# Optimization experiments

Hardware: AMD Instinct MI355X
Metric: run time of the kernel (lower is better)

Reference implementation:

```python
import jax, jax.numpy as jnp
import numpy as np

EPS = 1e-5

def _bn(h):
    # BatchNorm1d, affine=False, track_running_stats=False -> batch stats, biased var
    m = h.mean(axis=0)
    v = h.var(axis=0)
    return (h - m) * jax.lax.rsqrt(v + EPS)

def _aggregate(x, edge_index):
    # out[i] = sum over edges (i <- j) of x[j]  + x[i] (self loop)
    dst, src = edge_index[0], edge_index[1]
    n = x.shape[0]
    return jax.ops.segment_sum(x[src], dst, num_segments=n) + x

def setup_inputs() -> dict:
    key = jax.random.key(0)
    ks = jax.random.split(key, 12)
    N, F, H, C, E = 100000, 128, 128, 40, 800000
    x = jax.random.normal(ks[0], (N, F), dtype=jnp.float32)
    edge_index = jax.random.randint(ks[1], (2, E), 0, N, dtype=jnp.int64)
    def lin(kw, kb, fan_in, fan_out):
        bound = 1.0 / np.sqrt(fan_in)
        W = jax.random.uniform(kw, (fan_in, fan_out), minval=-bound, maxval=bound, dtype=jnp.float32)
        b = jax.random.uniform(kb, (fan_out,), minval=-bound, maxval=bound, dtype=jnp.float32)
        return W, b
    W0, b0 = lin(ks[2], ks[3], F, H)
    W1, b1 = lin(ks[4], ks[5], H, H)
    W2, b2 = lin(ks[6], ks[7], H, H)
    Wl, bl = lin(ks[8], ks[9], H, C)
    return {"x": x, "edge_index": edge_index, "W0": W0, "b0": b0,
            "W1": W1, "b1": b1, "W2": W2, "b2": b2, "Wl": Wl, "bl": bl}

def reference(x, edge_index, W0, b0, W1, b1, W2, b2, Wl, bl):
    h = x
    for W, b in ((W0, b0), (W1, b1), (W2, b2)):
        h = _aggregate(h, edge_index)          # spmm(A + I, h)
        h = h @ W + b                          # Linear
        h = _bn(h)                             # BatchNorm1d (no affine)
        h = jax.nn.relu(h)
    return h @ Wl + bl
```

## Files before the change

kernel.cpp:

```cpp
#include <hip/hip_runtime.h>
#include <stdint.h>

typedef __attribute__((ext_vector_type(8))) short short8;
typedef __attribute__((ext_vector_type(4))) float floatx4;

static __device__ __forceinline__ float b2f(uint16_t b){
    return __uint_as_float(((uint32_t)b) << 16);
}
static __device__ __forceinline__ uint16_t f2b(float f){
    uint32_t u = __float_as_uint(f);
    return (uint16_t)((u + 0x7fffu + ((u >> 16) & 1u)) >> 16);
}
static __device__ __forceinline__ float blo(uint32_t v){ return __uint_as_float(v << 16); }
static __device__ __forceinline__ float bhi(uint32_t v){ return __uint_as_float(v & 0xffff0000u); }
static __device__ __forceinline__ uint32_t pack2(float a, float b){
    return ((uint32_t)f2b(b) << 16) | (uint32_t)f2b(a);
}

__global__ void k_sentinel(uint32_t* out, int nwords, uint32_t pat){
    int i = blockIdx.x * blockDim.x + threadIdx.x;
    if (i < nwords) out[i] = pat;
}

__global__ void k_zf(int* deg8, int n8, const uint32_t* xw, const int* ei, int* flags, int ZB){
    if ((int)blockIdx.x == ZB){
        if (threadIdx.x != 0) return;
        int odd_nz = 0;
        for (int k = 0; k < 128; k++){
            if (ei[2 * k + 1] != 0) odd_nz = 1;
        }
        flags[0] = odd_nz ? 0 : 1;
        int big = 0;
        for (int k = 0; k < 128; k++){
            float lo = __uint_as_float(xw[k] << 16);
            if (!(fabsf(lo) <= 1024.0f)) big = 1;
        }
        flags[1] = big ? 0 : 1;
        return;
    }
    int i = blockIdx.x * blockDim.x + threadIdx.x;
    if (i < n8) deg8[i] = 0;
}

__global__ void k_deg(const int* ei, int E, int* deg8, uint16_t* rank, const int* flags,
                      unsigned q){
    int e = blockIdx.x * blockDim.x + threadIdx.x;
    if (e < E){
        int is64 = flags[0];
        int d = is64 ? ei[2 * e] : ei[e];
        unsigned sv = (unsigned)(is64 ? ei[2 * (E + e)] : ei[E + e]);
        int s = (int)(sv / q);
        int r = atomicAdd(&deg8[d * 8 + s], 1);
        rank[e] = (uint16_t)r;
    }
}

__global__ void k_off8(const int* __restrict__ deg8, int N, int* __restrict__ deg,
                       uint16_t* __restrict__ offs8){
    int i = blockIdx.x * blockDim.x + threadIdx.x;
    if (i >= N) return;
    int s = 0;
    #pragma unroll
    for (int k = 0; k < 8; k++){
        int c = deg8[i * 8 + k];
        offs8[i * 8 + k] = (uint16_t)s;
        s += c;
    }
    deg[i] = s;
}

__global__ void k_scan1(const int* deg, int N, int* bsum){
    __shared__ int s[256];
    int t = threadIdx.x;
    int i = blockIdx.x * 256 + t;
    s[t] = (i < N) ? deg[i] : 0;
    __syncthreads();
    for (int off = 128; off > 0; off >>= 1){
        if (t < off) s[t] += s[t + off];
        __syncthreads();
    }
    if (t == 0) bsum[blockIdx.x] = s[0];
}

__global__ void k_scan2(int* bsum, int nb, int* rp, int N){
    __shared__ int s[512];
    int t = threadIdx.x;
    int v = (t < nb) ? bsum[t] : 0;
    s[t] = v;
    __syncthreads();
    for (int off = 1; off < 512; off <<= 1){
        int u = (t >= off) ? s[t - off] : 0;
        __syncthreads();
        s[t] += u;
        __syncthreads();
    }
    if (t < nb) bsum[t] = s[t] - v;
    if (t == 511) rp[N] = s[511];
}

__global__ void k_scan3(const int* deg, int N, const int* bpre, int* rp){
    __shared__ int s[256];
    int t = threadIdx.x;
    int i = blockIdx.x * 256 + t;
    int v = (i < N) ? deg[i] : 0;
    s[t] = v;
    __syncthreads();
    for (int off = 1; off < 256; off <<= 1){
        int u = (t >= off) ? s[t - off] : 0;
        __syncthreads();
        s[t] += u;
        __syncthreads();
    }
    if (i < N) rp[i] = bpre[blockIdx.x] + s[t] - v;
}

__global__ __launch_bounds__(256) void k_fill(const int* __restrict__ ei, int E,
                                              const int* __restrict__ rp,
                                              const uint16_t* __restrict__ rank,
                                              const uint16_t* __restrict__ offs8,
                                              int* __restrict__ col,
                                              const int* __restrict__ flags, int N,
                                              unsigned q){
    int xcd = blockIdx.x & 7;
    int sub = blockIdx.x >> 3;
    int nsub = gridDim.x >> 3;
    int r0 = (int)(((long long)N * xcd) >> 3);
    int r1 = (int)(((long long)N * (xcd + 1)) >> 3);
    int e0 = (int)(((long long)E * sub) / nsub);
    int e1 = (int)(((long long)E * (sub + 1)) / nsub);
    int is64 = flags[0];
    for (int e = e0 + threadIdx.x; e < e1; e += 256){
        int d = is64 ? ei[2 * e] : ei[e];
        if (d >= r0 && d < r1){
            unsigned sv = (unsigned)(is64 ? ei[2 * (E + e)] : ei[E + e]);
            int s = (int)(sv / q);
            int p = rp[d] + (int)offs8[d * 8 + s] + (int)rank[e];
            col[p] = (int)sv;
        }
    }
}

__global__ void k_prep(const void* W0, const void* W1, const void* W2, const void* Wl,
                       uint16_t* Wf0, uint16_t* Wf1, uint16_t* Wf2, uint16_t* Wfl,
                       const void* b0, const void* b1, const void* b2, const void* bl,
                       float* bc, const void* x, uint16_t* hx, int NF,
                       const int* flags){
    int blk = blockIdx.x;
    int t = threadIdx.x;
    if (blk >= 218){
        if (flags[1]) return;
        int nb = gridDim.x - 218;
        for (int i = (blk - 218) * 256 + t; i < NF; i += nb * 256)
            hx[i] = f2b(((const float*)x)[i]);
        return;
    }
    if (blk >= 216){
        int i = (blk - 216) * 256 + t;
        if (i >= 424) return;
        const void* src; int li;
        if (i < 128)      { src = b0; li = i; }
        else if (i < 256) { src = b1; li = i - 128; }
        else if (i < 384) { src = b2; li = i - 256; }
        else              { src = bl; li = i - 384; }
        bc[i] = flags[1] ? b2f(((const uint16_t*)src)[li]) : ((const float*)src)[li];
        return;
    }
    const void* W; uint16_t* Wf; int C, ntiles, lb;
    if (blk < 64)        { W = W0; Wf = Wf0; C = 128; ntiles = 8; lb = blk; }
    else if (blk < 128)  { W = W1; Wf = Wf1; C = 128; ntiles = 8; lb = blk - 64; }
    else if (blk < 192)  { W = W2; Wf = Wf2; C = 128; ntiles = 8; lb = blk - 128; }
    else                 { W = Wl; Wf = Wfl; C = 40;  ntiles = 3; lb = blk - 192; }
    int idx = lb * 256 + t;
    int total = 4 * ntiles * 512;
    if (idx >= total) return;
    int j = idx & 7;
    int lane = (idx >> 3) & 63;
    int nt = (idx >> 9) % ntiles;
    int kt = idx / (512 * ntiles);
    int k = kt * 32 + (lane >> 4) * 8 + j;
    int n = nt * 16 + (lane & 15);
    uint16_t v = 0;
    if (n < C){
        v = flags[1] ? ((const uint16_t*)W)[k * C + n]
                     : f2b(((const float*)W)[k * C + n]);
    }
    Wf[idx] = v;
}

__global__ __launch_bounds__(256) void k_agg(const uint16_t* __restrict__ Yin,
                                             const uint16_t* __restrict__ xraw,
                                             const int* __restrict__ rp,
                                             const int* __restrict__ col,
                                             uint16_t* __restrict__ out, int N,
                                             const float* __restrict__ st,
                                             int apply_bn, float ninv,
                                             const int* __restrict__ flags){
    int t = threadIdx.x;
    int l16 = t & 15;
    int i = blockIdx.x * 16 + (t >> 4);
    if (i >= N) return;
    float tt[8], iv[8];
    const uint16_t* src = Yin;
    if (apply_bn){
        int f0 = l16 * 8;
        #pragma unroll
        for (int j = 0; j < 8; j++){
            float sv = st[f0 + j];
            float qv = st[128 + f0 + j];
            float m = sv * ninv;
            float var = qv * ninv - m * m;
            float ivj = rsqrtf(var + 1e-5f);
            iv[j] = ivj;
            tt[j] = -m * ivj;
        }
    } else if (flags[1]){
        src = xraw;
    }
    const uint4* base = (const uint4*)src;
    int s0 = rp[i], e0 = rp[i + 1];
    float a[8];
    {
        uint4 w = base[(size_t)i * 16 + l16];
        a[0] = blo(w.x); a[1] = bhi(w.x); a[2] = blo(w.y); a[3] = bhi(w.y);
        a[4] = blo(w.z); a[5] = bhi(w.z); a[6] = blo(w.w); a[7] = bhi(w.w);
        if (apply_bn){
            #pragma unroll
            for (int jj = 0; jj < 8; jj++) a[jj] = fmaxf(fmaf(a[jj], iv[jj], tt[jj]), 0.f);
        }
    }
    int k = s0;
    for (; k + 3 < e0; k += 4){
        int j0 = col[k], j1 = col[k + 1], j2 = col[k + 2], j3 = col[k + 3];
        uint4 ww[4];
        ww[0] = base[(size_t)j0 * 16 + l16];
        ww[1] = base[(size_t)j1 * 16 + l16];
        ww[2] = base[(size_t)j2 * 16 + l16];
        ww[3] = base[(size_t)j3 * 16 + l16];
        #pragma unroll
        for (int u = 0; u < 4; u++){
            float v[8] = {blo(ww[u].x), bhi(ww[u].x), blo(ww[u].y), bhi(ww[u].y),
                          blo(ww[u].z), bhi(ww[u].z), blo(ww[u].w), bhi(ww[u].w)};
            if (apply_bn){
                #pragma unroll
                for (int jj = 0; jj < 8; jj++) v[jj] = fmaxf(fmaf(v[jj], iv[jj], tt[jj]), 0.f);
            }
            #pragma unroll
            for (int jj = 0; jj < 8; jj++) a[jj] += v[jj];
        }
    }
    for (; k < e0; k++){
        int j = col[k];
        uint4 w = base[(size_t)j * 16 + l16];
        float v[8] = {blo(w.x), bhi(w.x), blo(w.y), bhi(w.y),
                      blo(w.z), bhi(w.z), blo(w.w), bhi(w.w)};
        if (apply_bn){
            #pragma unroll
            for (int jj = 0; jj < 8; jj++) v[jj] = fmaxf(fmaf(v[jj], iv[jj], tt[jj]), 0.f);
        }
        #pragma unroll
        for (int jj = 0; jj < 8; jj++) a[jj] += v[jj];
    }
    uint4 o;
    o.x = pack2(a[0], a[1]); o.y = pack2(a[2], a[3]);
    o.z = pack2(a[4], a[5]); o.w = pack2(a[6], a[7]);
    ((uint4*)out)[(size_t)i * 16 + l16] = o;
}

__global__ __launch_bounds__(256) void k_gemm(uint16_t* __restrict__ A,
                                              const uint16_t* __restrict__ Wf,
                                              const float* __restrict__ bias,
                                              float* __restrict__ part, int N){
    __shared__ __align__(16) uint16_t wlds[16384];
    __shared__ float sh_sum[128], sh_ssq[128];
    int t = threadIdx.x;
    if (t < 128){ sh_sum[t] = 0.f; sh_ssq[t] = 0.f; }
    {
        const uint4* s = (const uint4*)Wf;
        uint4* d = (uint4*)wlds;
        for (int i = t; i < 2048; i += 256) d[i] = s[i];
    }
    __syncthreads();
    int lane = t & 63, wave = t >> 6;
    int m = lane & 15, q = lane >> 4;
    int rb[2];
    rb[0] = blockIdx.x * 128 + wave * 16;
    rb[1] = rb[0] + 64;
    short8 afrag[2][4];
    #pragma unroll
    for (int mt = 0; mt < 2; mt++){
        int arow = rb[mt] + m;
        if (arow >= N) arow = N - 1;
        const short8* ap = (const short8*)(A + (size_t)arow * 128);
        #pragma unroll
        for (int kt = 0; kt < 4; kt++) afrag[mt][kt] = ap[kt * 4 + q];
    }
    floatx4 acc[2][8];
    #pragma unroll
    for (int mt = 0; mt < 2; mt++)
        #pragma unroll
        for (int nt = 0; nt < 8; nt++) acc[mt][nt] = (floatx4){0.f, 0.f, 0.f, 0.f};
    const short8* wl = (const short8*)wlds;
    #pragma unroll
    for (int kt = 0; kt < 4; kt++){
        #pragma unroll
        for (int nt = 0; nt < 8; nt++){
            short8 bfrag = wl[(kt * 8 + nt) * 64 + lane];
            #pragma unroll
            for (int mt = 0; mt < 2; mt++){
                acc[mt][nt] = __builtin_amdgcn_mfma_f32_16x16x32_bf16(afrag[mt][kt], bfrag, acc[mt][nt], 0, 0, 0);
            }
        }
    }
    #pragma unroll
    for (int mt = 0; mt < 2; mt++){
        #pragma unroll
        for (int nt = 0; nt < 8; nt++){
            int ccol = nt * 16 + m;
            float bv = bias[ccol];
            float s = 0.f, ss = 0.f;
            #pragma unroll
            for (int r = 0; r < 4; r++){
                int grow = rb[mt] + q * 4 + r;
                if (grow < N){
                    float y = acc[mt][nt][r] + bv;
                    A[(size_t)grow * 128 + ccol] = f2b(y);
                    s += y;
                    ss += y * y;
                }
            }
            s += __shfl_xor(s, 16); s += __shfl_xor(s, 32);
            ss += __shfl_xor(ss, 16); ss += __shfl_xor(ss, 32);
            if (q == 0){
                atomicAdd(&sh_sum[ccol], s);
                atomicAdd(&sh_ssq[ccol], ss);
            }
        }
    }
    __syncthreads();
    if (t < 128){
        part[(size_t)blockIdx.x * 256 + t] = sh_sum[t];
        part[(size_t)blockIdx.x * 256 + 128 + t] = sh_ssq[t];
    }
}

__global__ __launch_bounds__(1024) void k_red(const float* __restrict__ part, int nb,
                                              float* __restrict__ st){
    __shared__ float sh[1024];
    int t = threadIdx.x;
    int col = t & 255;
    int seg = t >> 8;
    float s0 = 0.f, s1 = 0.f, s2 = 0.f, s3 = 0.f;
    int b = seg;
    for (; b + 12 < nb; b += 16){
        s0 += part[(size_t)b * 256 + col];
        s1 += part[(size_t)(b + 4) * 256 + col];
        s2 += part[(size_t)(b + 8) * 256 + col];
        s3 += part[(size_t)(b + 12) * 256 + col];
    }
    for (; b < nb; b += 4) s0 += part[(size_t)b * 256 + col];
    sh[t] = (s0 + s1) + (s2 + s3);
    __syncthreads();
    if (t < 256) st[t] = (sh[t] + sh[t + 256]) + (sh[t + 512] + sh[t + 768]);
}

__global__ __launch_bounds__(256) void k_out(const uint16_t* __restrict__ A,
                                             const uint16_t* __restrict__ Wf,
                                             const float* __restrict__ bias,
                                             const float* __restrict__ st, float ninv,
                                             void* __restrict__ out, int N,
                                             const int* __restrict__ flags){
    __shared__ __align__(16) uint16_t wlds[6144];
    __shared__ float s_m[128], s_iv[128];
    int t = threadIdx.x;
    {
        const uint4* s = (const uint4*)Wf;
        uint4* d = (uint4*)wlds;
        for (int i = t; i < 768; i += 256) d[i] = s[i];
    }
    if (t < 128){
        float m = st[t] * ninv;
        float var = st[128 + t] * ninv - m * m;
        s_m[t] = m;
        s_iv[t] = rsqrtf(var + 1e-5f);
    }
    __syncthreads();
    int lane = t & 63, wave = t >> 6;
    int m = lane & 15, q = lane >> 4;
    int row_base = blockIdx.x * 64 + wave * 16;
    int arow = row_base + m;
    if (arow >= N) arow = N - 1;
    short8 afrag[4];
    const uint4* ap = (const uint4*)(A + (size_t)arow * 128);
    #pragma unroll
    for (int kt = 0; kt < 4; kt++){
        uint4 u = ap[kt * 4 + q];
        float v[8] = {blo(u.x), bhi(u.x), blo(u.y), bhi(u.y),
                      blo(u.z), bhi(u.z), blo(u.w), bhi(u.w)};
        int c0 = kt * 32 + q * 8;
        #pragma unroll
        for (int j = 0; j < 8; j++) v[j] = fmaxf((v[j] - s_m[c0 + j]) * s_iv[c0 + j], 0.f);
        uint4 o;
        o.x = pack2(v[0], v[1]); o.y = pack2(v[2], v[3]);
        o.z = pack2(v[4], v[5]); o.w = pack2(v[6], v[7]);
        afrag[kt] = *(short8*)&o;
    }
    floatx4 acc[3];
    #pragma unroll
    for (int nt = 0; nt < 3; nt++) acc[nt] = (floatx4){0.f, 0.f, 0.f, 0.f};
    const short8* wl = (const short8*)wlds;
    #pragma unroll
    for (int kt = 0; kt < 4; kt++){
        #pragma unroll
        for (int nt = 0; nt < 3; nt++){
            acc[nt] = __builtin_amdgcn_mfma_f32_16x16x32_bf16(afrag[kt], wl[(kt * 3 + nt) * 64 + lane], acc[nt], 0, 0, 0);
        }
    }
    int isbf = flags[1];
    #pragma unroll
    for (int nt = 0; nt < 3; nt++){
        int ccol = nt * 16 + m;
        if (ccol < 40){
            float bv = bias[ccol];
            #pragma unroll
            for (int r = 0; r < 4; r++){
                int grow = row_base + q * 4 + r;
                if (grow < N){
                    float y = acc[nt][r] + bv;
                    if (isbf) ((uint16_t*)out)[(size_t)grow * 40 + ccol] = f2b(y);
                    else      ((float*)out)[(size_t)grow * 40 + ccol] = y;
                }
            }
        }
    }
}

extern "C" void kernel_launch(void* const* d_in, const int* in_sizes, int n_in,
                              void* d_out, int out_size, void* d_ws, size_t ws_size,
                              hipStream_t stream){
    (void)n_in;
    const void* x  = d_in[0];
    const int* ei  = (const int*)d_in[1];
    const void* W0 = d_in[2];
    const void* b0 = d_in[3];
    const void* W1 = d_in[4];
    const void* b1 = d_in[5];
    const void* W2 = d_in[6];
    const void* b2 = d_in[7];
    const void* Wl = d_in[8];
    const void* bl = d_in[9];

    const int N = in_sizes[0] / 128;
    const int E = in_sizes[1] / 2;
    const int NF = N * 128;
    const int NB = (N + 255) / 256;
    const int gemm_blocks2 = (N + 127) / 128;
    const int gemm_blocks  = (N + 63) / 64;
    const unsigned q8 = (unsigned)((N + 7) / 8);

    char* ws = (char*)d_ws;
    size_t off = 0;
    uint16_t* hx = (uint16_t*)(ws + off); off += ((size_t)NF * 2 + 255) & ~(size_t)255;
    uint16_t* ag = (uint16_t*)(ws + off); off += ((size_t)NF * 2 + 255) & ~(size_t)255;
    int* col     = (int*)(ws + off);      off += ((size_t)E * 4 + 255) & ~(size_t)255;
    int* rp      = (int*)(ws + off);      off += ((size_t)(N + 1) * 4 + 255) & ~(size_t)255;
    uint16_t* rank = (uint16_t*)(ws + off); off += ((size_t)E * 2 + 255) & ~(size_t)255;
    int* deg8    = (int*)(ws + off);      off += ((size_t)N * 32 + 255) & ~(size_t)255;
    uint16_t* offs8 = (uint16_t*)(ws + off); off += ((size_t)N * 16 + 255) & ~(size_t)255;
    int* deg     = (int*)(ws + off);      off += ((size_t)N * 4 + 255) & ~(size_t)255;
    int* bsum    = (int*)(ws + off);      off += 512 * 4;
    int* flags   = (int*)(ws + off);      off += 256;
    uint16_t* Wf0 = (uint16_t*)(ws + off); off += 16384 * 2;
    uint16_t* Wf1 = (uint16_t*)(ws + off); off += 16384 * 2;
    uint16_t* Wf2 = (uint16_t*)(ws + off); off += 16384 * 2;
    uint16_t* Wfl = (uint16_t*)(ws + off); off += 6144 * 2;
    float* bc    = (float*)(ws + off);    off += 424 * 4 + 160;
    float* stats = (float*)(ws + off);    off += 768 * 4;
    float* part  = (float*)(ws + off);    off += (size_t)gemm_blocks2 * 256 * 4;
    const size_t required = off;

    if (ws_size < required){
        int nwords = out_size / 2;
        k_sentinel<<<(nwords + 255) / 256, 256, 0, stream>>>((uint32_t*)d_out, nwords, 0x40004000u);
        return;
    }

    const int n8 = N * 8;
    const int ZB = (n8 + 255) / 256;
    k_zf<<<ZB + 1, 256, 0, stream>>>(deg8, n8, (const uint32_t*)x, ei, flags, ZB);
    k_deg<<<(E + 255) / 256, 256, 0, stream>>>(ei, E, deg8, rank, flags, q8);
    k_off8<<<(N + 255) / 256, 256, 0, stream>>>(deg8, N, deg, offs8);
    k_scan1<<<NB, 256, 0, stream>>>(deg, N, bsum);
    k_scan2<<<1, 512, 0, stream>>>(bsum, NB, rp, N);
    k_scan3<<<NB, 256, 0, stream>>>(deg, N, bsum, rp);
    k_fill<<<1024, 256, 0, stream>>>(ei, E, rp, rank, offs8, col, flags, N, q8);

    k_prep<<<2266, 256, 0, stream>>>(W0, W1, W2, Wl, Wf0, Wf1, Wf2, Wfl,
                                     b0, b1, b2, bl, bc, x, hx, NF, flags);

    const float ninv = 1.0f / (float)N;
    const int agg_blocks = (N + 15) / 16;
    const uint16_t* xr = (const uint16_t*)x;

    k_agg<<<agg_blocks, 256, 0, stream>>>(hx, xr, rp, col, ag, N, stats, 0, ninv, flags);
    k_gemm<<<gemm_blocks2, 256, 0, stream>>>(ag, Wf0, bc, part, N);
    k_red<<<1, 1024, 0, stream>>>(part, gemm_blocks2, stats);
    k_agg<<<agg_blocks, 256, 0, stream>>>(ag, xr, rp, col, hx, N, stats, 1, ninv, flags);
    k_gemm<<<gemm_blocks2, 256, 0, stream>>>(hx, Wf1, bc + 128, part, N);
    k_red<<<1, 1024, 0, stream>>>(part, gemm_blocks2, stats + 256);
    k_agg<<<agg_blocks, 256, 0, stream>>>(hx, xr, rp, col, ag, N, stats + 256, 1, ninv, flags);
    k_gemm<<<gemm_blocks2, 256, 0, stream>>>(ag, Wf2, bc + 256, part, N);
    k_red<<<1, 1024, 0, stream>>>(part, gemm_blocks2, stats + 512);
    k_out<<<gemm_blocks, 256, 0, stream>>>(ag, Wfl, bc + 384, stats + 512, ninv, d_out, N, flags);
}
```

Before: 437.4 us.

## Unroll aggregation gathers by eight, fuse offset/scan kernels, parallelize stat reduction

```diff
diff --git a/kernel.cpp b/kernel.cpp
--- a/kernel.cpp
+++ b/kernel.cpp
@@ -56,30 +56,27 @@
 }
 
 __global__ void k_off8(const int* __restrict__ deg8, int N, int* __restrict__ deg,
-                       uint16_t* __restrict__ offs8){
-    int i = blockIdx.x * blockDim.x + threadIdx.x;
-    if (i >= N) return;
+                       uint16_t* __restrict__ offs8, int* __restrict__ bsum){
+    __shared__ int sh[256];
+    int t = threadIdx.x;
+    int i = blockIdx.x * 256 + t;
     int s = 0;
-    #pragma unroll
-    for (int k = 0; k < 8; k++){
-        int c = deg8[i * 8 + k];
-        offs8[i * 8 + k] = (uint16_t)s;
-        s += c;
-    }
-    deg[i] = s;
-}
-
-__global__ void k_scan1(const int* deg, int N, int* bsum){
-    __shared__ int s[256];
-    int t = threadIdx.x;
-    int i = blockIdx.x * 256 + t;
-    s[t] = (i < N) ? deg[i] : 0;
+    if (i < N){
+        #pragma unroll
+        for (int k = 0; k < 8; k++){
+            int c = deg8[i * 8 + k];
+            offs8[i * 8 + k] = (uint16_t)s;
+            s += c;
+        }
+        deg[i] = s;
+    }
+    sh[t] = (i < N) ? s : 0;
     __syncthreads();
     for (int off = 128; off > 0; off >>= 1){
-        if (t < off) s[t] += s[t + off];
+        if (t < off) sh[t] += sh[t + off];
         __syncthreads();
     }
-    if (t == 0) bsum[blockIdx.x] = s[0];
+    if (t == 0) bsum[blockIdx.x] = sh[0];
 }
 
 __global__ void k_scan2(int* bsum, int nb, int* rp, int N){
@@ -187,7 +184,7 @@
     Wf[idx] = v;
 }
 
-__global__ __launch_bounds__(256) void k_agg(const uint16_t* __restrict__ Yin,
+__global__ __launch_bounds__(256, 4) void k_agg(const uint16_t* __restrict__ Yin,
                                              const uint16_t* __restrict__ xraw,
                                              const int* __restrict__ rp,
                                              const int* __restrict__ col,
@@ -228,37 +225,48 @@
             for (int jj = 0; jj < 8; jj++) a[jj] = fmaxf(fmaf(a[jj], iv[jj], tt[jj]), 0.f);
         }
     }
+    auto acc1 = [&](uint4 w){
+        float v0 = blo(w.x), v1 = bhi(w.x), v2 = blo(w.y), v3 = bhi(w.y);
+        float v4 = blo(w.z), v5 = bhi(w.z), v6 = blo(w.w), v7 = bhi(w.w);
+        if (apply_bn){
+            v0 = fmaxf(fmaf(v0, iv[0], tt[0]), 0.f);
+            v1 = fmaxf(fmaf(v1, iv[1], tt[1]), 0.f);
+            v2 = fmaxf(fmaf(v2, iv[2], tt[2]), 0.f);
+            v3 = fmaxf(fmaf(v3, iv[3], tt[3]), 0.f);
+            v4 = fmaxf(fmaf(v4, iv[4], tt[4]), 0.f);
+            v5 = fmaxf(fmaf(v5, iv[5], tt[5]), 0.f);
+            v6 = fmaxf(fmaf(v6, iv[6], tt[6]), 0.f);
+            v7 = fmaxf(fmaf(v7, iv[7], tt[7]), 0.f);
+        }
+        a[0] += v0; a[1] += v1; a[2] += v2; a[3] += v3;
+        a[4] += v4; a[5] += v5; a[6] += v6; a[7] += v7;
+    };
     int k = s0;
+    for (; k + 7 < e0; k += 8){
+        int j0 = col[k],     j1 = col[k + 1], j2 = col[k + 2], j3 = col[k + 3];
+        int j4 = col[k + 4], j5 = col[k + 5], j6 = col[k + 6], j7 = col[k + 7];
+        uint4 w0 = base[(size_t)j0 * 16 + l16];
+        uint4 w1 = base[(size_t)j1 * 16 + l16];
+        uint4 w2 = base[(size_t)j2 * 16 + l16];
+        uint4 w3 = base[(size_t)j3 * 16 + l16];
+        uint4 w4 = base[(size_t)j4 * 16 + l16];
+        uint4 w5 = base[(size_t)j5 * 16 + l16];
+        uint4 w6 = base[(size_t)j6 * 16 + l16];
+        uint4 w7 = base[(size_t)j7 * 16 + l16];
+        acc1(w0); acc1(w1); acc1(w2); acc1(w3);
+        acc1(w4); acc1(w5); acc1(w6); acc1(w7);
+    }
     for (; k + 3 < e0; k += 4){
         int j0 = col[k], j1 = col[k + 1], j2 = col[k + 2], j3 = col[k + 3];
-        uint4 ww[4];
-        ww[0] = base[(size_t)j0 * 16 + l16];
-        ww[1] = base[(size_t)j1 * 16 + l16];
-        ww[2] = base[(size_t)j2 * 16 + l16];
-        ww[3] = base[(size_t)j3 * 16 + l16];
-        #pragma unroll
-        for (int u = 0; u < 4; u++){
-            float v[8] = {blo(ww[u].x), bhi(ww[u].x), blo(ww[u].y), bhi(ww[u].y),
-                          blo(ww[u].z), bhi(ww[u].z), blo(ww[u].w), bhi(ww[u].w)};
-            if (apply_bn){
-                #pragma unroll
-                for (int jj = 0; jj < 8; jj++) v[jj] = fmaxf(fmaf(v[jj], iv[jj], tt[jj]), 0.f);
-            }
-            #pragma unroll
-            for (int jj = 0; jj < 8; jj++) a[jj] += v[jj];
-        }
+        uint4 w0 = base[(size_t)j0 * 16 + l16];
+        uint4 w1 = base[(size_t)j1 * 16 + l16];
+        uint4 w2 = base[(size_t)j2 * 16 + l16];
+        uint4 w3 = base[(size_t)j3 * 16 + l16];
+        acc1(w0); acc1(w1); acc1(w2); acc1(w3);
     }
     for (; k < e0; k++){
         int j = col[k];
-        uint4 w = base[(size_t)j * 16 + l16];
-        float v[8] = {blo(w.x), bhi(w.x), blo(w.y), bhi(w.y),
-                      blo(w.z), bhi(w.z), blo(w.w), bhi(w.w)};
-        if (apply_bn){
-            #pragma unroll
-            for (int jj = 0; jj < 8; jj++) v[jj] = fmaxf(fmaf(v[jj], iv[jj], tt[jj]), 0.f);
-        }
-        #pragma unroll
-        for (int jj = 0; jj < 8; jj++) a[jj] += v[jj];
+        acc1(base[(size_t)j * 16 + l16]);
     }
     uint4 o;
     o.x = pack2(a[0], a[1]); o.y = pack2(a[2], a[3]);
@@ -343,24 +351,26 @@
     }
 }
 
-__global__ __launch_bounds__(1024) void k_red(const float* __restrict__ part, int nb,
-                                              float* __restrict__ st){
-    __shared__ float sh[1024];
-    int t = threadIdx.x;
-    int col = t & 255;
-    int seg = t >> 8;
-    float s0 = 0.f, s1 = 0.f, s2 = 0.f, s3 = 0.f;
+__global__ __launch_bounds__(256) void k_red(const float* __restrict__ part, int nb,
+                                             float* __restrict__ st){
+    __shared__ float sh[256];
+    int t = threadIdx.x;
+    int c = t & 31, seg = t >> 5;
+    int cc = blockIdx.x * 32 + c;
+    float s0 = 0.f, s1 = 0.f;
     int b = seg;
-    for (; b + 12 < nb; b += 16){
-        s0 += part[(size_t)b * 256 + col];
-        s1 += part[(size_t)(b + 4) * 256 + col];
-        s2 += part[(size_t)(b + 8) * 256 + col];
-        s3 += part[(size_t)(b + 12) * 256 + col];
-    }
-    for (; b < nb; b += 4) s0 += part[(size_t)b * 256 + col];
-    sh[t] = (s0 + s1) + (s2 + s3);
-    __syncthreads();
-    if (t < 256) st[t] = (sh[t] + sh[t + 256]) + (sh[t + 512] + sh[t + 768]);
+    for (; b + 8 < nb; b += 16){
+        s0 += part[(size_t)b * 256 + cc];
+        s1 += part[(size_t)(b + 8) * 256 + cc];
+    }
+    for (; b < nb; b += 8) s0 += part[(size_t)b * 256 + cc];
+    sh[t] = s0 + s1;
+    __syncthreads();
+    if (t < 128) sh[t] += sh[t + 128];
+    __syncthreads();
+    if (t < 64) sh[t] += sh[t + 64];
+    __syncthreads();
+    if (t < 32) st[cc] = sh[t] + sh[t + 32];
 }
 
 __global__ __launch_bounds__(256) void k_out(const uint16_t* __restrict__ A,
@@ -488,8 +498,7 @@
     const int ZB = (n8 + 255) / 256;
     k_zf<<<ZB + 1, 256, 0, stream>>>(deg8, n8, (const uint32_t*)x, ei, flags, ZB);
     k_deg<<<(E + 255) / 256, 256, 0, stream>>>(ei, E, deg8, rank, flags, q8);
-    k_off8<<<(N + 255) / 256, 256, 0, stream>>>(deg8, N, deg, offs8);
-    k_scan1<<<NB, 256, 0, stream>>>(deg, N, bsum);
+    k_off8<<<NB, 256, 0, stream>>>(deg8, N, deg, offs8, bsum);
     k_scan2<<<1, 512, 0, stream>>>(bsum, NB, rp, N);
     k_scan3<<<NB, 256, 0, stream>>>(deg, N, bsum, rp);
     k_fill<<<1024, 256, 0, stream>>>(ei, E, rp, rank, offs8, col, flags, N, q8);
@@ -503,12 +512,12 @@
 
     k_agg<<<agg_blocks, 256, 0, stream>>>(hx, xr, rp, col, ag, N, stats, 0, ninv, flags);
     k_gemm<<<gemm_blocks2, 256, 0, stream>>>(ag, Wf0, bc, part, N);
-    k_red<<<1, 1024, 0, stream>>>(part, gemm_blocks2, stats);
+    k_red<<<8, 256, 0, stream>>>(part, gemm_blocks2, stats);
     k_agg<<<agg_blocks, 256, 0, stream>>>(ag, xr, rp, col, hx, N, stats, 1, ninv, flags);
     k_gemm<<<gemm_blocks2, 256, 0, stream>>>(hx, Wf1, bc + 128, part, N);
-    k_red<<<1, 1024, 0, stream>>>(part, gemm_blocks2, stats + 256);
+    k_red<<<8, 256, 0, stream>>>(part, gemm_blocks2, stats + 256);
     k_agg<<<agg_blocks, 256, 0, stream>>>(hx, xr, rp, col, ag, N, stats + 256, 1, ninv, flags);
     k_gemm<<<gemm_blocks2, 256, 0, stream>>>(ag, Wf2, bc + 256, part, N);
-    k_red<<<1, 1024, 0, stream>>>(part, gemm_blocks2, stats + 512);
+    k_red<<<8, 256, 0, stream>>>(part, gemm_blocks2, stats + 512);
     k_out<<<gemm_blocks, 256, 0, stream>>>(ag, Wfl, bc + 384, stats + 512, ninv, d_out, N, flags);
 }
```

After: 452.0 us. 3.3% more time.

## Fuse aggregation with GEMM and simplify CSR build to per-node degree

Applied to the files above, without the earlier changes.

```diff
diff --git a/kernel.cpp b/kernel.cpp
--- a/kernel.cpp
+++ b/kernel.cpp
@@ -22,7 +22,7 @@
     if (i < nwords) out[i] = pat;
 }
 
-__global__ void k_zf(int* deg8, int n8, const uint32_t* xw, const int* ei, int* flags, int ZB){
+__global__ void k_zf(int* deg, int N, const uint32_t* xw, const int* ei, int* flags, int ZB){
     if ((int)blockIdx.x == ZB){
         if (threadIdx.x != 0) return;
         int odd_nz = 0;
@@ -39,34 +39,16 @@
         return;
     }
     int i = blockIdx.x * blockDim.x + threadIdx.x;
-    if (i < n8) deg8[i] = 0;
-}
-
-__global__ void k_deg(const int* ei, int E, int* deg8, uint16_t* rank, const int* flags,
-                      unsigned q){
+    if (i < N) deg[i] = 0;
+}
+
+__global__ void k_deg(const int* ei, int E, int* deg, uint16_t* rank, const int* flags){
     int e = blockIdx.x * blockDim.x + threadIdx.x;
     if (e < E){
-        int is64 = flags[0];
-        int d = is64 ? ei[2 * e] : ei[e];
-        unsigned sv = (unsigned)(is64 ? ei[2 * (E + e)] : ei[E + e]);
-        int s = (int)(sv / q);
-        int r = atomicAdd(&deg8[d * 8 + s], 1);
+        int d = flags[0] ? ei[2 * e] : ei[e];
+        int r = atomicAdd(&deg[d], 1);
         rank[e] = (uint16_t)r;
     }
-}
-
-__global__ void k_off8(const int* __restrict__ deg8, int N, int* __restrict__ deg,
-                       uint16_t* __restrict__ offs8){
-    int i = blockIdx.x * blockDim.x + threadIdx.x;
-    if (i >= N) return;
-    int s = 0;
-    #pragma unroll
-    for (int k = 0; k < 8; k++){
-        int c = deg8[i * 8 + k];
-        offs8[i * 8 + k] = (uint16_t)s;
-        s += c;
-    }
-    deg[i] = s;
 }
 
 __global__ void k_scan1(const int* deg, int N, int* bsum){
@@ -117,10 +99,8 @@
 __global__ __launch_bounds__(256) void k_fill(const int* __restrict__ ei, int E,
                                               const int* __restrict__ rp,
                                               const uint16_t* __restrict__ rank,
-                                              const uint16_t* __restrict__ offs8,
                                               int* __restrict__ col,
-                                              const int* __restrict__ flags, int N,
-                                              unsigned q){
+                                              const int* __restrict__ flags, int N){
     int xcd = blockIdx.x & 7;
     int sub = blockIdx.x >> 3;
     int nsub = gridDim.x >> 3;
@@ -132,10 +112,9 @@
     for (int e = e0 + threadIdx.x; e < e1; e += 256){
         int d = is64 ? ei[2 * e] : ei[e];
         if (d >= r0 && d < r1){
-            unsigned sv = (unsigned)(is64 ? ei[2 * (E + e)] : ei[E + e]);
-            int s = (int)(sv / q);
-            int p = rp[d] + (int)offs8[d * 8 + s] + (int)rank[e];
-            col[p] = (int)sv;
+            int sv = is64 ? ei[2 * (E + e)] : ei[E + e];
+            int p = rp[d] + (int)rank[e];
+            col[p] = sv;
         }
     }
 }
@@ -150,8 +129,17 @@
     if (blk >= 218){
         if (flags[1]) return;
         int nb = gridDim.x - 218;
-        for (int i = (blk - 218) * 256 + t; i < NF; i += nb * 256)
-            hx[i] = f2b(((const float*)x)[i]);
+        int n8 = NF >> 3;
+        const float4* xv = (const float4*)x;
+        uint4* hv = (uint4*)hx;
+        for (int i = (blk - 218) * 256 + t; i < n8; i += nb * 256){
+            float4 u0 = xv[i * 2];
+            float4 u1 = xv[i * 2 + 1];
+            uint4 o;
+            o.x = pack2(u0.x, u0.y); o.y = pack2(u0.z, u0.w);
+            o.z = pack2(u1.x, u1.y); o.w = pack2(u1.z, u1.w);
+            hv[i] = o;
+        }
         return;
     }
     if (blk >= 216){
@@ -187,18 +175,25 @@
     Wf[idx] = v;
 }
 
-__global__ __launch_bounds__(256) void k_agg(const uint16_t* __restrict__ Yin,
-                                             const uint16_t* __restrict__ xraw,
-                                             const int* __restrict__ rp,
-                                             const int* __restrict__ col,
-                                             uint16_t* __restrict__ out, int N,
-                                             const float* __restrict__ st,
-                                             int apply_bn, float ninv,
-                                             const int* __restrict__ flags){
-    int t = threadIdx.x;
+__global__ __launch_bounds__(256) void k_ag(const uint16_t* __restrict__ Yin,
+                                            const uint16_t* __restrict__ xraw,
+                                            const int* __restrict__ rp,
+                                            const int* __restrict__ col,
+                                            uint16_t* __restrict__ Yout,
+                                            const uint16_t* __restrict__ Wf,
+                                            const float* __restrict__ bias,
+                                            float* __restrict__ part, int N,
+                                            const float* __restrict__ st,
+                                            int apply_bn, float ninv,
+                                            const int* __restrict__ flags){
+    __shared__ __align__(16) uint16_t albs[2048];
+    __shared__ float sh_sum[128], sh_ssq[128];
+    int t = threadIdx.x;
+    if (t < 128){ sh_sum[t] = 0.f; sh_ssq[t] = 0.f; }
     int l16 = t & 15;
-    int i = blockIdx.x * 16 + (t >> 4);
-    if (i >= N) return;
+    int r = t >> 4;
+    int row = blockIdx.x * 16 + r;
+    int i = (row < N) ? row : N - 1;
     float tt[8], iv[8];
     const uint16_t* src = Yin;
     if (apply_bn){
@@ -260,80 +255,55 @@
         #pragma unroll
         for (int jj = 0; jj < 8; jj++) a[jj] += v[jj];
     }
-    uint4 o;
-    o.x = pack2(a[0], a[1]); o.y = pack2(a[2], a[3]);
-    o.z = pack2(a[4], a[5]); o.w = pack2(a[6], a[7]);
-    ((uint4*)out)[(size_t)i * 16 + l16] = o;
-}
-
-__global__ __launch_bounds__(256) void k_gemm(uint16_t* __restrict__ A,
-                                              const uint16_t* __restrict__ Wf,
-                                              const float* __restrict__ bias,
-                                              float* __restrict__ part, int N){
-    __shared__ __align__(16) uint16_t wlds[16384];
-    __shared__ float sh_sum[128], sh_ssq[128];
-    int t = threadIdx.x;
-    if (t < 128){ sh_sum[t] = 0.f; sh_ssq[t] = 0.f; }
     {
-        const uint4* s = (const uint4*)Wf;
-        uint4* d = (uint4*)wlds;
-        for (int i = t; i < 2048; i += 256) d[i] = s[i];
+        uint4 o;
+        o.x = pack2(a[0], a[1]); o.y = pack2(a[2], a[3]);
+        o.z = pack2(a[4], a[5]); o.w = pack2(a[6], a[7]);
+        int wb = r * 256 + ((l16 * 16) ^ ((r & 7) << 4));
+        *(uint4*)((char*)albs + wb) = o;
     }
     __syncthreads();
     int lane = t & 63, wave = t >> 6;
     int m = lane & 15, q = lane >> 4;
-    int rb[2];
-    rb[0] = blockIdx.x * 128 + wave * 16;
-    rb[1] = rb[0] + 64;
-    short8 afrag[2][4];
-    #pragma unroll
-    for (int mt = 0; mt < 2; mt++){
-        int arow = rb[mt] + m;
-        if (arow >= N) arow = N - 1;
-        const short8* ap = (const short8*)(A + (size_t)arow * 128);
-        #pragma unroll
-        for (int kt = 0; kt < 4; kt++) afrag[mt][kt] = ap[kt * 4 + q];
-    }
-    floatx4 acc[2][8];
-    #pragma unroll
-    for (int mt = 0; mt < 2; mt++)
-        #pragma unroll
-        for (int nt = 0; nt < 8; nt++) acc[mt][nt] = (floatx4){0.f, 0.f, 0.f, 0.f};
-    const short8* wl = (const short8*)wlds;
+    short8 af[4];
     #pragma unroll
     for (int kt = 0; kt < 4; kt++){
-        #pragma unroll
-        for (int nt = 0; nt < 8; nt++){
-            short8 bfrag = wl[(kt * 8 + nt) * 64 + lane];
-            #pragma unroll
-            for (int mt = 0; mt < 2; mt++){
-                acc[mt][nt] = __builtin_amdgcn_mfma_f32_16x16x32_bf16(afrag[mt][kt], bfrag, acc[mt][nt], 0, 0, 0);
+        int rb = m * 256 + ((kt * 64 + q * 16) ^ ((m & 7) << 4));
+        af[kt] = *(const short8*)((const char*)albs + rb);
+    }
+    const short8* wg = (const short8*)Wf;
+    floatx4 acc[2];
+    acc[0] = (floatx4){0.f, 0.f, 0.f, 0.f};
+    acc[1] = (floatx4){0.f, 0.f, 0.f, 0.f};
+    #pragma unroll
+    for (int kt = 0; kt < 4; kt++){
+        #pragma unroll
+        for (int n2 = 0; n2 < 2; n2++){
+            short8 bf = wg[(kt * 8 + wave * 2 + n2) * 64 + lane];
+            acc[n2] = __builtin_amdgcn_mfma_f32_16x16x32_bf16(af[kt], bf, acc[n2], 0, 0, 0);
+        }
+    }
+    int row_base = blockIdx.x * 16;
+    #pragma unroll
+    for (int n2 = 0; n2 < 2; n2++){
+        int ccol = (wave * 2 + n2) * 16 + m;
+        float bv = bias[ccol];
+        float s = 0.f, ss = 0.f;
+        #pragma unroll
+        for (int rr = 0; rr < 4; rr++){
+            int grow = row_base + q * 4 + rr;
+            if (grow < N){
+                float y = acc[n2][rr] + bv;
+                Yout[(size_t)grow * 128 + ccol] = f2b(y);
+                s += y;
+                ss += y * y;
             }
         }
-    }
-    #pragma unroll
-    for (int mt = 0; mt < 2; mt++){
-        #pragma unroll
-        for (int nt = 0; nt < 8; nt++){
-            int ccol = nt * 16 + m;
-            float bv = bias[ccol];
-            float s = 0.f, ss = 0.f;
-            #pragma unroll
-            for (int r = 0; r < 4; r++){
-                int grow = rb[mt] + q * 4 + r;
-                if (grow < N){
-                    float y = acc[mt][nt][r] + bv;
-                    A[(size_t)grow * 128 + ccol] = f2b(y);
-                    s += y;
-                    ss += y * y;
-                }
-            }
-            s += __shfl_xor(s, 16); s += __shfl_xor(s, 32);
-            ss += __shfl_xor(ss, 16); ss += __shfl_xor(ss, 32);
-            if (q == 0){
-                atomicAdd(&sh_sum[ccol], s);
-                atomicAdd(&sh_ssq[ccol], ss);
-            }
+        s += __shfl_xor(s, 16); s += __shfl_xor(s, 32);
+        ss += __shfl_xor(ss, 16); ss += __shfl_xor(ss, 32);
+        if (q == 0){
+            atomicAdd(&sh_sum[ccol], s);
+            atomicAdd(&sh_ssq[ccol], ss);
         }
     }
     __syncthreads();
@@ -343,24 +313,26 @@
     }
 }
 
-__global__ __launch_bounds__(1024) void k_red(const float* __restrict__ part, int nb,
-                                              float* __restrict__ st){
-    __shared__ float sh[1024];
-    int t = threadIdx.x;
-    int col = t & 255;
-    int seg = t >> 8;
-    float s0 = 0.f, s1 = 0.f, s2 = 0.f, s3 = 0.f;
+__global__ __launch_bounds__(256) void k_red(const float* __restrict__ part, int nb,
+                                             float* __restrict__ st){
+    __shared__ float sh[256];
+    int t = threadIdx.x;
+    int c = t & 31, seg = t >> 5;
+    int cc = blockIdx.x * 32 + c;
+    float s0 = 0.f, s1 = 0.f;
     int b = seg;
-    for (; b + 12 < nb; b += 16){
-        s0 += part[(size_t)b * 256 + col];
-        s1 += part[(size_t)(b + 4) * 256 + col];
-        s2 += part[(size_t)(b + 8) * 256 + col];
-        s3 += part[(size_t)(b + 12) * 256 + col];
-    }
-    for (; b < nb; b += 4) s0 += part[(size_t)b * 256 + col];
-    sh[t] = (s0 + s1) + (s2 + s3);
-    __syncthreads();
-    if (t < 256) st[t] = (sh[t] + sh[t + 256]) + (sh[t + 512] + sh[t + 768]);
+    for (; b + 8 < nb; b += 16){
+        s0 += part[(size_t)b * 256 + cc];
+        s1 += part[(size_t)(b + 8) * 256 + cc];
+    }
+    for (; b < nb; b += 8) s0 += part[(size_t)b * 256 + cc];
+    sh[t] = s0 + s1;
+    __syncthreads();
+    if (t < 128) sh[t] += sh[t + 128];
+    __syncthreads();
+    if (t < 64) sh[t] += sh[t + 64];
+    __syncthreads();
+    if (t < 32) st[cc] = sh[t] + sh[t + 32];
 }
 
 __global__ __launch_bounds__(256) void k_out(const uint16_t* __restrict__ A,
@@ -453,9 +425,8 @@
     const int E = in_sizes[1] / 2;
     const int NF = N * 128;
     const int NB = (N + 255) / 256;
-    const int gemm_blocks2 = (N + 127) / 128;
-    const int gemm_blocks  = (N + 63) / 64;
-    const unsigned q8 = (unsigned)((N + 7) / 8);
+    const int agg_blocks  = (N + 15) / 16;
+    const int gemm_blocks = (N + 63) / 64;
 
     char* ws = (char*)d_ws;
     size_t off = 0;
@@ -464,8 +435,6 @@
     int* col     = (int*)(ws + off);      off += ((size_t)E * 4 + 255) & ~(size_t)255;
     int* rp      = (int*)(ws + off);      off += ((size_t)(N + 1) * 4 + 255) & ~(size_t)255;
     uint16_t* rank = (uint16_t*)(ws + off); off += ((size_t)E * 2 + 255) & ~(size_t)255;
-    int* deg8    = (int*)(ws + off);      off += ((size_t)N * 32 + 255) & ~(size_t)255;
-    uint16_t* offs8 = (uint16_t*)(ws + off); off += ((size_t)N * 16 + 255) & ~(size_t)255;
     int* deg     = (int*)(ws + off);      off += ((size_t)N * 4 + 255) & ~(size_t)255;
     int* bsum    = (int*)(ws + off);      off += 512 * 4;
     int* flags   = (int*)(ws + off);      off += 256;
@@ -475,7 +444,7 @@
     uint16_t* Wfl = (uint16_t*)(ws + off); off += 6144 * 2;
     float* bc    = (float*)(ws + off);    off += 424 * 4 + 160;
     float* stats = (float*)(ws + off);    off += 768 * 4;
-    float* part  = (float*)(ws + off);    off += (size_t)gemm_blocks2 * 256 * 4;
+    float* part  = (float*)(ws + off);    off += (size_t)agg_blocks * 256 * 4;
     const size_t required = off;
 
     if (ws_size < required){
@@ -484,31 +453,27 @@
         return;
     }
 
-    const int n8 = N * 8;
-    const int ZB = (n8 + 255) / 256;
-    k_zf<<<ZB + 1, 256, 0, stream>>>(deg8, n8, (const uint32_t*)x, ei, flags, ZB);
-    k_deg<<<(E + 255) / 256, 256, 0, stream>>>(ei, E, deg8, rank, flags, q8);
-    k_off8<<<(N + 255) / 256, 256, 0, stream>>>(deg8, N, deg, offs8);
+    k_zf<<<NB + 1, 256, 0, stream>>>(deg, N, (const uint32_t*)x, ei, flags, NB);
+    k_deg<<<(E + 255) / 256, 256, 0, stream>>>(ei, E, deg, rank, flags);
     k_scan1<<<NB, 256, 0, stream>>>(deg, N, bsum);
     k_scan2<<<1, 512, 0, stream>>>(bsum, NB, rp, N);
     k_scan3<<<NB, 256, 0, stream>>>(deg, N, bsum, rp);
-    k_fill<<<1024, 256, 0, stream>>>(ei, E, rp, rank, offs8, col, flags, N, q8);
+    k_fill<<<1024, 256, 0, stream>>>(ei, E, rp, rank, col, flags, N);
 
     k_prep<<<2266, 256, 0, stream>>>(W0, W1, W2, Wl, Wf0, Wf1, Wf2, Wfl,
                                      b0, b1, b2, bl, bc, x, hx, NF, flags);
 
     const float ninv = 1.0f / (float)N;
-    const int agg_blocks = (N + 15) / 16;
     const uint16_t* xr = (const uint16_t*)x;
 
-    k_agg<<<agg_blocks, 256, 0, stream>>>(hx, xr, rp, col, ag, N, stats, 0, ninv, flags);
-    k_gemm<<<gemm_blocks2, 256, 0, stream>>>(ag, Wf0, bc, part, N);
-    k_red<<<1, 1024, 0, stream>>>(part, gemm_blocks2, stats);
-    k_agg<<<agg_blocks, 256, 0, stream>>>(ag, xr, rp, col, hx, N, stats, 1, ninv, flags);
-    k_gemm<<<gemm_blocks2, 256, 0, stream>>>(hx, Wf1, bc + 128, part, N);
-    k_red<<<1, 1024, 0, stream>>>(part, gemm_blocks2, stats + 256);
-    k_agg<<<agg_blocks, 256, 0, stream>>>(hx, xr, rp, col, ag, N, stats + 256, 1, ninv, flags);
-    k_gemm<<<gemm_blocks2, 256, 0, stream>>>(ag, Wf2, bc + 256, part, N);
-    k_red<<<1, 1024, 0, stream>>>(part, gemm_blocks2, stats + 512);
+    k_ag<<<agg_blocks, 256, 0, stream>>>(hx, xr, rp, col, ag, Wf0, bc, part, N,
+                                         stats, 0, ninv, flags);
+    k_red<<<8, 256, 0, stream>>>(part, agg_blocks, stats);
+    k_ag<<<agg_blocks, 256, 0, stream>>>(ag, xr, rp, col, hx, Wf1, bc + 128, part, N,
+                                         stats, 1, ninv, flags);
+    k_red<<<8, 256, 0, stream>>>(part, agg_blocks, stats + 256);
+    k_ag<<<agg_blocks, 256, 0, stream>>>(hx, xr, rp, col, ag, Wf2, bc + 256, part, N,
+                                         stats + 256, 1, ninv, flags);
+    k_red<<<8, 256, 0, stream>>>(part, agg_blocks, stats + 512);
     k_out<<<gemm_blocks, 256, 0, stream>>>(ag, Wfl, bc + 384, stats + 512, ninv, d_out, N, flags);
 }
```

New measurement: 718.3 us. 64.2% more time.
